# Performance work log

Measured on AMD Instinct MI355X. Metric: run time of the kernel, lower is better.

The kernel has to match this reference:

```python
import jax, jax.numpy as jnp
import numpy as np
import math, functools

QUERY_DIM = 64
HEADS = 4
DIM_HEAD = 16
INNER_DIM = HEADS * DIM_HEAD  # 64


def setup_inputs() -> dict:
    key = jax.random.key(0)
    k0, k1, k2, k3, k4, k5 = jax.random.split(key, 6)
    B, N, H = 4, 4096, 8
    s = 1.0 / math.sqrt(QUERY_DIM)
    return {
        "x": jax.random.normal(k0, (B, N, H, QUERY_DIM), dtype=jnp.float32),
        "Wq": jax.random.normal(k1, (QUERY_DIM, INNER_DIM), dtype=jnp.float32) * s,
        "Wk": jax.random.normal(k2, (QUERY_DIM, INNER_DIM), dtype=jnp.float32) * s,
        "Wv": jax.random.normal(k3, (QUERY_DIM, INNER_DIM), dtype=jnp.float32) * s,
        "Wo": jax.random.normal(k4, (INNER_DIM, QUERY_DIM), dtype=jnp.float32) * s,
        "bo": jnp.zeros((QUERY_DIM,), dtype=jnp.float32),
    }


def _query_chunk_size(n: int) -> int:
    # mirrors the module's chunk-size selection on flatten_latent_dim = shape[-3]
    if n % 64 == 0:
        return n // 64
    if n % 16 == 0:
        return n // 16
    if n % 4 == 0:
        return n // 4
    return n


def _chunked_attention(q, k, v, q_chunk):
    # q,k,v: (..., seq, h, d). Online-softmax chunking over queries; key_chunk_size
    # (16384) exceeds num_kv so a single key chunk is used -> per-q-chunk softmax
    # over the full key axis, which is exactly the same math as the original
    # max-rescaled accumulation.
    prec = jax.lax.Precision.HIGHEST
    scale = 1.0 / math.sqrt(k.shape[-1])
    q = q * scale
    nq = q.shape[-3]

    @functools.partial(jax.checkpoint, prevent_cse=False)
    def one_chunk(i):
        qc = jax.lax.dynamic_slice_in_dim(q, i, q_chunk, axis=-3)  # (..., qc, h, d)
        s = jnp.einsum('...qhd,...khd->...qhk', qc, k, precision=prec)
        a = jax.nn.softmax(s, axis=-1)  # stable: single max-subtract
        return jnp.einsum('...khf,...qhk->...qhf', v, a, precision=prec)

    res = jax.lax.map(one_chunk, jnp.arange(0, nq, q_chunk))  # (nchunks, ..., qc, h, f)
    return jnp.concatenate(res, axis=-3)  # (..., nq, h, f)


def reference(x, Wq, Wk, Wv, Wo, bo):
    # context = x (self-attention path)
    q = jnp.einsum('...d,df->...f', x, Wq)
    k = jnp.einsum('...d,df->...f', x, Wk)
    v = jnp.einsum('...d,df->...f', x, Wv)
    qcs = _query_chunk_size(q.shape[-3])
    hidden = _chunked_attention(q, k, v, qcs)
    return jnp.einsum('...f,fd->...d', hidden, Wo) + bo
```

## Files before the change

### kernel.cpp

```cpp
#include <hip/hip_runtime.h>
#include <hip/hip_bf16.h>

typedef __attribute__((ext_vector_type(8))) short short8;
typedef __attribute__((ext_vector_type(4))) float f32x4;
typedef __attribute__((ext_vector_type(8))) unsigned short ushort8;
typedef __attribute__((ext_vector_type(2))) unsigned uint2v;

#define LOG2E 1.44269504088896340736f

__device__ __forceinline__ float fexp2(float x) {
#if __has_builtin(__builtin_amdgcn_exp2f)
  return __builtin_amdgcn_exp2f(x);
#else
  return exp2f(x);
#endif
}
__device__ __forceinline__ unsigned cvtpk(float lo, float hi) {
  unsigned r;
  asm("v_cvt_pk_bf16_f32 %0, %1, %2" : "=v"(r) : "v"(lo), "v"(hi));
  return r;
}
__device__ __forceinline__ void pswap32(unsigned &a, unsigned &b) {
#if __has_builtin(__builtin_amdgcn_permlane32_swap)
  uint2v r = __builtin_amdgcn_permlane32_swap(a, b, false, false);
  a = r[0]; b = r[1];
#else
  asm("v_permlane32_swap_b32 %0, %1" : "+v"(a), "+v"(b));
#endif
}
__device__ __forceinline__ void gload_lds16(const unsigned short* g, unsigned short* l) {
  __builtin_amdgcn_global_load_lds(
      (const __attribute__((address_space(1))) unsigned int*)g,
      (__attribute__((address_space(3))) unsigned int*)l, 16, 0, 0);
}
__device__ __forceinline__ int swzK(int r) {
  return ((r & 3) | (((r >> 3) & 1) << 2)) << 3;
}

__global__ __launch_bounds__(256) void proj_kernel(
    const float* __restrict__ x,
    const float* __restrict__ Wq, const float* __restrict__ Wk,
    const float* __restrict__ Wv,
    unsigned short* __restrict__ Qo, unsigned short* __restrict__ Ko,
    unsigned short* __restrict__ Vto)
{
  const int tid = threadIdx.x, lane = tid & 63, w = tid >> 6;
  const int r15 = lane & 15, G = lane >> 4;
  const int bh = blockIdx.x >> 4, nt = blockIdx.x & 15;
  const int b = bh >> 3, h = bh & 7;
  const int n0 = nt * 256 + w * 64;

  short8 xf[4][2];
  #pragma unroll
  for (int ct = 0; ct < 4; ++ct) {
    const int n = n0 + ct * 16 + r15;
    const float* xr = x + ((size_t)((b * 4096 + n) * 8 + h)) * 64;
    #pragma unroll
    for (int s = 0; s < 2; ++s) {
      const f32x4 f0 = *(const f32x4*)&xr[s * 32 + G * 8];
      const f32x4 f1 = *(const f32x4*)&xr[s * 32 + G * 8 + 4];
      union { unsigned u[4]; short8 s8; } uu;
      uu.u[0] = cvtpk(f0[0], f0[1]); uu.u[1] = cvtpk(f0[2], f0[3]);
      uu.u[2] = cvtpk(f1[0], f1[1]); uu.u[3] = cvtpk(f1[2], f1[3]);
      xf[ct][s] = uu.s8;
    }
  }

  const size_t obase = (size_t)bh * (4096 * 64);

  #pragma unroll
  for (int wi = 0; wi < 2; ++wi) {
    const float* W = wi ? Wk : Wq;
    unsigned short* O = wi ? Ko : Qo;
    const float sc = wi ? 1.0f : 0.125f * LOG2E;
    short8 wf[4][2];
    #pragma unroll
    for (int ft = 0; ft < 4; ++ft)
      #pragma unroll
      for (int s = 0; s < 2; ++s) {
        union { unsigned u[4]; short8 s8; } uu;
        #pragma unroll
        for (int jj = 0; jj < 4; ++jj) {
          const int k0 = s * 32 + G * 8 + jj * 2;
          uu.u[jj] = cvtpk(W[k0 * 64 + ft * 16 + r15] * sc,
                           W[(k0 + 1) * 64 + ft * 16 + r15] * sc);
        }
        wf[ft][s] = uu.s8;
      }
    f32x4 acc[4][4];
    #pragma unroll
    for (int ft = 0; ft < 4; ++ft)
      #pragma unroll
      for (int ct = 0; ct < 4; ++ct) acc[ft][ct] = (f32x4){0.f, 0.f, 0.f, 0.f};
    #pragma unroll
    for (int s = 0; s < 2; ++s)
      #pragma unroll
      for (int ft = 0; ft < 4; ++ft)
        #pragma unroll
        for (int ct = 0; ct < 4; ++ct)
          acc[ft][ct] = __builtin_amdgcn_mfma_f32_16x16x32_bf16(
              wf[ft][s], xf[ct][s], acc[ft][ct], 0, 0, 0);
    #pragma unroll
    for (int ft = 0; ft < 4; ++ft)
      #pragma unroll
      for (int ct = 0; ct < 4; ++ct) {
        uint2v pk;
        pk[0] = cvtpk(acc[ft][ct][0], acc[ft][ct][1]);
        pk[1] = cvtpk(acc[ft][ct][2], acc[ft][ct][3]);
        *(uint2v*)&O[obase + (size_t)(n0 + ct * 16 + r15) * 64 + ft * 16 + G * 4] = pk;
      }
  }

  {
    short8 wf[4][2];
    #pragma unroll
    for (int ft = 0; ft < 4; ++ft)
      #pragma unroll
      for (int s = 0; s < 2; ++s) {
        union { unsigned u[4]; short8 s8; } uu;
        #pragma unroll
        for (int jj = 0; jj < 4; ++jj) {
          const int k0 = s * 32 + G * 8 + jj * 2;
          uu.u[jj] = cvtpk(Wv[k0 * 64 + ft * 16 + r15], Wv[(k0 + 1) * 64 + ft * 16 + r15]);
        }
        wf[ft][s] = uu.s8;
      }
    f32x4 acc[4][4];
    #pragma unroll
    for (int ct = 0; ct < 4; ++ct)
      #pragma unroll
      for (int ft = 0; ft < 4; ++ft) acc[ct][ft] = (f32x4){0.f, 0.f, 0.f, 0.f};
    #pragma unroll
    for (int s = 0; s < 2; ++s)
      #pragma unroll
      for (int ct = 0; ct < 4; ++ct)
        #pragma unroll
        for (int ft = 0; ft < 4; ++ft)
          acc[ct][ft] = __builtin_amdgcn_mfma_f32_16x16x32_bf16(
              xf[ct][s], wf[ft][s], acc[ct][ft], 0, 0, 0);
    #pragma unroll
    for (int ct = 0; ct < 4; ++ct)
      #pragma unroll
      for (int ft = 0; ft < 4; ++ft) {
        uint2v pk;
        pk[0] = cvtpk(acc[ct][ft][0], acc[ct][ft][1]);
        pk[1] = cvtpk(acc[ct][ft][2], acc[ct][ft][3]);
        *(uint2v*)&Vto[obase + (size_t)(ft * 16 + r15) * 4096 + n0 + ct * 16 + G * 4] = pk;
      }
  }
}

__global__ __launch_bounds__(256, 4) void attn_kernel(
    const unsigned short* __restrict__ Q, const unsigned short* __restrict__ K,
    const unsigned short* __restrict__ Vt, const float* __restrict__ Wo,
    const float* __restrict__ bo, float* __restrict__ out)
{
  __shared__ __align__(16) unsigned short SM[16384];

  const int tid = threadIdx.x;
  const int lane = tid & 63, w = tid >> 6;
  const int r15 = lane & 15, G = lane >> 4;

  int bid = blockIdx.x;
  bid = (bid & 7) * 128 + (bid >> 3);
  const int bh = bid >> 5, qt128 = bid & 31;

  const unsigned short* Qb = Q + (size_t)bh * (4096 * 64);
  const unsigned short* Kb = K + (size_t)bh * (4096 * 64);
  const unsigned short* Vb = Vt + (size_t)bh * (64 * 4096);
  const int q0w = qt128 * 128 + w * 32;

  short8 qf[2][2];
  #pragma unroll
  for (int qt = 0; qt < 2; ++qt) {
    const unsigned short* qr = Qb + (size_t)(q0w + qt * 16 + r15) * 64;
    qf[qt][0] = *(const short8*)&qr[G * 8];
    qf[qt][1] = *(const short8*)&qr[32 + G * 8];
  }

  short8 ones8;
  {
    union { unsigned short us[8]; short8 s8; } o;
    #pragma unroll
    for (int i = 0; i < 8; ++i) o.us[i] = 0x3F80;
    ones8 = o.s8;
  }

  f32x4 oacc[2][4];
  #pragma unroll
  for (int qt = 0; qt < 2; ++qt)
    #pragma unroll
    for (int t = 0; t < 4; ++t) oacc[qt][t] = (f32x4){0.f, 0.f, 0.f, 0.f};
  f32x4 lacc[2];
  lacc[0] = (f32x4){0.f, 0.f, 0.f, 0.f};
  lacc[1] = (f32x4){0.f, 0.f, 0.f, 0.f};

  int kro[4][2], vro[4][2];
  {
    const int Rr = r15 >> 2, gg = r15 & 3;
    #pragma unroll
    for (int t = 0; t < 4; ++t) {
      const int row = gg + ((t & 1) << 2) + ((Rr & 1) << 3) + ((t >> 1) << 4) + ((Rr >> 1) << 5);
      const int sw = swzK(row);
      kro[t][0] = row * 64 + ((G * 8) ^ sw);
      kro[t][1] = row * 64 + ((32 + G * 8) ^ sw);
      const int vrow = t * 16 + r15;
      const int vs = (vrow & 7) << 3;
      vro[t][0] = vrow * 64 + ((G * 8) ^ vs);
      vro[t][1] = vrow * 64 + ((32 + G * 8) ^ vs);
    }
  }

  const int seg = w * 2;
  const int kr0 = seg * 8 + (lane >> 3), kr1 = kr0 + 8;
  const int c8 = (lane & 7) * 8;
  const int koff0 = kr0 * 64 + (c8 ^ swzK(kr0));
  const int koff1 = kr1 * 64 + (c8 ^ swzK(kr1));
  const int voff0 = kr0 * 4096 + (c8 ^ ((kr0 & 7) << 3));
  const int voff1 = kr1 * 4096 + (c8 ^ ((kr1 & 7) << 3));

  gload_lds16(Kb + koff0, &SM[seg * 512]);
  gload_lds16(Kb + koff1, &SM[(seg + 1) * 512]);
  gload_lds16(Vb + voff0, &SM[8192 + seg * 512]);
  gload_lds16(Vb + voff1, &SM[8192 + (seg + 1) * 512]);
  __syncthreads();

  auto TILE = [&](int bufc, int ktc) {
    if (ktc < 63) {
      const int ko = (ktc + 1) * 4096;
      const int vo = (ktc + 1) * 64;
      unsigned short* kd = &SM[(bufc ^ 1) * 4096];
      unsigned short* vd = &SM[8192 + (bufc ^ 1) * 4096];
      gload_lds16(Kb + ko + koff0, kd + seg * 512);
      gload_lds16(Kb + ko + koff1, kd + (seg + 1) * 512);
      gload_lds16(Vb + vo + voff0, vd + seg * 512);
      gload_lds16(Vb + vo + voff1, vd + (seg + 1) * 512);
    }

    const unsigned short* Kc = &SM[bufc * 4096];
    const unsigned short* Vc = &SM[8192 + bufc * 4096];

    f32x4 s[2][4];
    #pragma unroll
    for (int t = 0; t < 4; ++t) {
      const short8 kf0 = *(const short8*)&Kc[kro[t][0]];
      const short8 kf1 = *(const short8*)&Kc[kro[t][1]];
      f32x4 z0 = (f32x4){0.f, 0.f, 0.f, 0.f};
      f32x4 z1 = (f32x4){0.f, 0.f, 0.f, 0.f};
      z0 = __builtin_amdgcn_mfma_f32_16x16x32_bf16(kf0, qf[0][0], z0, 0, 0, 0);
      s[0][t] = __builtin_amdgcn_mfma_f32_16x16x32_bf16(kf1, qf[0][1], z0, 0, 0, 0);
      z1 = __builtin_amdgcn_mfma_f32_16x16x32_bf16(kf0, qf[1][0], z1, 0, 0, 0);
      s[1][t] = __builtin_amdgcn_mfma_f32_16x16x32_bf16(kf1, qf[1][1], z1, 0, 0, 0);
    }

    short8 pa[2][2];
    #pragma unroll
    for (int qt = 0; qt < 2; ++qt) {
      float p[4][4];
      #pragma unroll
      for (int t = 0; t < 4; ++t)
        #pragma unroll
        for (int g = 0; g < 4; ++g) p[t][g] = fexp2(s[qt][t][g]);

      unsigned wA[4], wB[4];
      wA[0] = cvtpk(p[0][0], p[0][1]); wA[1] = cvtpk(p[0][2], p[0][3]);
      wA[2] = cvtpk(p[1][0], p[1][1]); wA[3] = cvtpk(p[1][2], p[1][3]);
      wB[0] = cvtpk(p[2][0], p[2][1]); wB[1] = cvtpk(p[2][2], p[2][3]);
      wB[2] = cvtpk(p[3][0], p[3][1]); wB[3] = cvtpk(p[3][2], p[3][3]);
      union { unsigned u[4]; short8 s8; } fa, fb;
      #pragma unroll
      for (int i = 0; i < 4; ++i) {
        pswap32(wA[i], wB[i]);
        fa.u[i] = wA[i];
        fb.u[i] = wB[i];
      }
      pa[qt][0] = fa.s8;
      pa[qt][1] = fb.s8;
    }

    lacc[0] = __builtin_amdgcn_mfma_f32_16x16x32_bf16(pa[0][0], ones8, lacc[0], 0, 0, 0);
    lacc[0] = __builtin_amdgcn_mfma_f32_16x16x32_bf16(pa[0][1], ones8, lacc[0], 0, 0, 0);
    lacc[1] = __builtin_amdgcn_mfma_f32_16x16x32_bf16(pa[1][0], ones8, lacc[1], 0, 0, 0);
    lacc[1] = __builtin_amdgcn_mfma_f32_16x16x32_bf16(pa[1][1], ones8, lacc[1], 0, 0, 0);

    #pragma unroll
    for (int t = 0; t < 4; ++t) {
      const short8 vb0 = *(const short8*)&Vc[vro[t][0]];
      const short8 vb1 = *(const short8*)&Vc[vro[t][1]];
      oacc[0][t] = __builtin_amdgcn_mfma_f32_16x16x32_bf16(pa[0][0], vb0, oacc[0][t], 0, 0, 0);
      oacc[0][t] = __builtin_amdgcn_mfma_f32_16x16x32_bf16(pa[0][1], vb1, oacc[0][t], 0, 0, 0);
      oacc[1][t] = __builtin_amdgcn_mfma_f32_16x16x32_bf16(pa[1][0], vb0, oacc[1][t], 0, 0, 0);
      oacc[1][t] = __builtin_amdgcn_mfma_f32_16x16x32_bf16(pa[1][1], vb1, oacc[1][t], 0, 0, 0);
    }
    __syncthreads();
  };

  for (int kt = 0; kt < 64; kt += 2) {
    TILE(0, kt);
    TILE(1, kt + 1);
  }

  float* Ol = (float*)&SM[0] + w * 2048;
  #pragma unroll
  for (int qt = 0; qt < 2; ++qt) {
    float li[4];
    #pragma unroll
    for (int g = 0; g < 4; ++g) li[g] = __builtin_amdgcn_rcpf(lacc[qt][g]);
    #pragma unroll
    for (int t = 0; t < 4; ++t)
      #pragma unroll
      for (int g = 0; g < 4; ++g) {
        const int q = qt * 16 + G * 4 + g;
        const int d = t * 16 + r15;
        Ol[q * 64 + (d ^ ((q & 7) << 3))] = oacc[qt][t][g] * li[g];
      }
  }

  short8 wof[4][2];
  #pragma unroll
  for (int nt = 0; nt < 4; ++nt)
    #pragma unroll
    for (int st = 0; st < 2; ++st) {
      union { unsigned u[4]; short8 s8; } uu;
      #pragma unroll
      for (int jj = 0; jj < 4; ++jj) {
        const int k0 = st * 32 + G * 8 + jj * 2;
        uu.u[jj] = cvtpk(Wo[k0 * 64 + nt * 16 + r15], Wo[(k0 + 1) * 64 + nt * 16 + r15]);
      }
      wof[nt][st] = uu.s8;
    }
  float bov[4];
  #pragma unroll
  for (int nt = 0; nt < 4; ++nt) bov[nt] = bo[nt * 16 + r15];

  const int b = bh >> 3, hh = bh & 7;
  #pragma unroll
  for (int qt2 = 0; qt2 < 2; ++qt2) {
    short8 af[2];
    #pragma unroll
    for (int st = 0; st < 2; ++st) {
      const int row = qt2 * 16 + r15;
      const int c = (st * 32 + G * 8) ^ ((row & 7) << 3);
      const f32x4 f0 = *(const f32x4*)&Ol[row * 64 + c];
      const f32x4 f1 = *(const f32x4*)&Ol[row * 64 + c + 4];
      union { unsigned u[4]; short8 s8; } uu;
      uu.u[0] = cvtpk(f0[0], f0[1]); uu.u[1] = cvtpk(f0[2], f0[3]);
      uu.u[2] = cvtpk(f1[0], f1[1]); uu.u[3] = cvtpk(f1[2], f1[3]);
      af[st] = uu.s8;
    }
    #pragma unroll
    for (int nt = 0; nt < 4; ++nt) {
      f32x4 dacc = (f32x4){bov[nt], bov[nt], bov[nt], bov[nt]};
      dacc = __builtin_amdgcn_mfma_f32_16x16x32_bf16(af[0], wof[nt][0], dacc, 0, 0, 0);
      dacc = __builtin_amdgcn_mfma_f32_16x16x32_bf16(af[1], wof[nt][1], dacc, 0, 0, 0);
      #pragma unroll
      for (int g = 0; g < 4; ++g) {
        const int nq = q0w + qt2 * 16 + G * 4 + g;
        out[((size_t)(b * 4096 + nq) * 8 + hh) * 64 + nt * 16 + r15] = dacc[g];
      }
    }
  }
}

extern "C" void kernel_launch(void* const* d_in, const int* in_sizes, int n_in,
                              void* d_out, int out_size, void* d_ws, size_t ws_size,
                              hipStream_t stream) {
  const float* x  = (const float*)d_in[0];
  const float* Wq = (const float*)d_in[1];
  const float* Wk = (const float*)d_in[2];
  const float* Wv = (const float*)d_in[3];
  const float* Wo = (const float*)d_in[4];
  const float* bo = (const float*)d_in[5];

  const size_t NE = 8388608;
  unsigned short* Qw  = (unsigned short*)d_ws;
  unsigned short* Kw  = Qw + NE;
  unsigned short* Vtw = Kw + NE;

  proj_kernel<<<512, 256, 0, stream>>>(x, Wq, Wk, Wv, Qw, Kw, Vtw);
  attn_kernel<<<1024, 256, 0, stream>>>(Qw, Kw, Vtw, Wo, bo, (float*)d_out);
}
```

Measured before the change: 173.3 us.

## Switch attention inner loop to 32x32x16 MFMA tiles with new LDS swizzle

Rewrites the attention kernel's QK^T, row-sum and PV matmuls to use 32x32x16 bf16 MFMA instructions instead of 16x16x32, with each wave handling a full 32-query tile. The K layout swizzle and fragment offsets are redone to match the new operand layout, and launch bounds drop from 4 to 3 waves per SIMD to allow the larger 16-float accumulators. The aim is fewer MFMA issues and LDS reads per tile, traded against higher register pressure and lower occupancy.

```diff
diff --git a/kernel.cpp b/kernel.cpp
--- a/kernel.cpp
+++ b/kernel.cpp
@@ -3,6 +3,7 @@
 
 typedef __attribute__((ext_vector_type(8))) short short8;
 typedef __attribute__((ext_vector_type(4))) float f32x4;
+typedef __attribute__((ext_vector_type(16))) float f32x16;
 typedef __attribute__((ext_vector_type(8))) unsigned short ushort8;
 typedef __attribute__((ext_vector_type(2))) unsigned uint2v;
 
@@ -32,9 +33,6 @@
   __builtin_amdgcn_global_load_lds(
       (const __attribute__((address_space(1))) unsigned int*)g,
       (__attribute__((address_space(3))) unsigned int*)l, 16, 0, 0);
-}
-__device__ __forceinline__ int swzK(int r) {
-  return ((r & 3) | (((r >> 3) & 1) << 2)) << 3;
 }
 
 __global__ __launch_bounds__(256) void proj_kernel(
@@ -150,7 +148,7 @@
   }
 }
 
-__global__ __launch_bounds__(256, 4) void attn_kernel(
+__global__ __launch_bounds__(256, 3) void attn_kernel(
     const unsigned short* __restrict__ Q, const unsigned short* __restrict__ K,
     const unsigned short* __restrict__ Vt, const float* __restrict__ Wo,
     const float* __restrict__ bo, float* __restrict__ out)
@@ -159,6 +157,7 @@
 
   const int tid = threadIdx.x;
   const int lane = tid & 63, w = tid >> 6;
+  const int l31 = lane & 31, hi = lane >> 5;
   const int r15 = lane & 15, G = lane >> 4;
 
   int bid = blockIdx.x;
@@ -170,12 +169,11 @@
   const unsigned short* Vb = Vt + (size_t)bh * (64 * 4096);
   const int q0w = qt128 * 128 + w * 32;
 
-  short8 qf[2][2];
-  #pragma unroll
-  for (int qt = 0; qt < 2; ++qt) {
-    const unsigned short* qr = Qb + (size_t)(q0w + qt * 16 + r15) * 64;
-    qf[qt][0] = *(const short8*)&qr[G * 8];
-    qf[qt][1] = *(const short8*)&qr[32 + G * 8];
+  short8 qf[4];
+  {
+    const unsigned short* qr = Qb + (size_t)(q0w + l31) * 64;
+    #pragma unroll
+    for (int s = 0; s < 4; ++s) qf[s] = *(const short8*)&qr[s * 16 + hi * 8];
   }
 
   short8 ones8;
@@ -186,36 +184,23 @@
     ones8 = o.s8;
   }
 
-  f32x4 oacc[2][4];
-  #pragma unroll
-  for (int qt = 0; qt < 2; ++qt)
-    #pragma unroll
-    for (int t = 0; t < 4; ++t) oacc[qt][t] = (f32x4){0.f, 0.f, 0.f, 0.f};
-  f32x4 lacc[2];
-  lacc[0] = (f32x4){0.f, 0.f, 0.f, 0.f};
-  lacc[1] = (f32x4){0.f, 0.f, 0.f, 0.f};
-
-  int kro[4][2], vro[4][2];
+  f32x16 oacc[2];
+  f32x16 lacc;
+  #pragma unroll
+  for (int r = 0; r < 16; ++r) { oacc[0][r] = 0.f; oacc[1][r] = 0.f; lacc[r] = 0.f; }
+
+  int roffE[4];
   {
-    const int Rr = r15 >> 2, gg = r15 & 3;
-    #pragma unroll
-    for (int t = 0; t < 4; ++t) {
-      const int row = gg + ((t & 1) << 2) + ((Rr & 1) << 3) + ((t >> 1) << 4) + ((Rr >> 1) << 5);
-      const int sw = swzK(row);
-      kro[t][0] = row * 64 + ((G * 8) ^ sw);
-      kro[t][1] = row * 64 + ((32 + G * 8) ^ sw);
-      const int vrow = t * 16 + r15;
-      const int vs = (vrow & 7) << 3;
-      vro[t][0] = vrow * 64 + ((G * 8) ^ vs);
-      vro[t][1] = vrow * 64 + ((32 + G * 8) ^ vs);
-    }
+    const int m = hi ^ (l31 & 7);
+    #pragma unroll
+    for (int s = 0; s < 4; ++s) roffE[s] = l31 * 64 + ((s * 2) ^ m) * 8;
   }
 
   const int seg = w * 2;
   const int kr0 = seg * 8 + (lane >> 3), kr1 = kr0 + 8;
   const int c8 = (lane & 7) * 8;
-  const int koff0 = kr0 * 64 + (c8 ^ swzK(kr0));
-  const int koff1 = kr1 * 64 + (c8 ^ swzK(kr1));
+  const int koff0 = kr0 * 64 + (c8 ^ ((kr0 & 7) << 3));
+  const int koff1 = kr1 * 64 + (c8 ^ ((kr1 & 7) << 3));
   const int voff0 = kr0 * 4096 + (c8 ^ ((kr0 & 7) << 3));
   const int voff1 = kr1 * 4096 + (c8 ^ ((kr1 & 7) << 3));
 
@@ -240,58 +225,43 @@
     const unsigned short* Kc = &SM[bufc * 4096];
     const unsigned short* Vc = &SM[8192 + bufc * 4096];
 
-    f32x4 s[2][4];
-    #pragma unroll
-    for (int t = 0; t < 4; ++t) {
-      const short8 kf0 = *(const short8*)&Kc[kro[t][0]];
-      const short8 kf1 = *(const short8*)&Kc[kro[t][1]];
-      f32x4 z0 = (f32x4){0.f, 0.f, 0.f, 0.f};
-      f32x4 z1 = (f32x4){0.f, 0.f, 0.f, 0.f};
-      z0 = __builtin_amdgcn_mfma_f32_16x16x32_bf16(kf0, qf[0][0], z0, 0, 0, 0);
-      s[0][t] = __builtin_amdgcn_mfma_f32_16x16x32_bf16(kf1, qf[0][1], z0, 0, 0, 0);
-      z1 = __builtin_amdgcn_mfma_f32_16x16x32_bf16(kf0, qf[1][0], z1, 0, 0, 0);
-      s[1][t] = __builtin_amdgcn_mfma_f32_16x16x32_bf16(kf1, qf[1][1], z1, 0, 0, 0);
-    }
-
-    short8 pa[2][2];
-    #pragma unroll
-    for (int qt = 0; qt < 2; ++qt) {
-      float p[4][4];
-      #pragma unroll
-      for (int t = 0; t < 4; ++t)
-        #pragma unroll
-        for (int g = 0; g < 4; ++g) p[t][g] = fexp2(s[qt][t][g]);
-
-      unsigned wA[4], wB[4];
-      wA[0] = cvtpk(p[0][0], p[0][1]); wA[1] = cvtpk(p[0][2], p[0][3]);
-      wA[2] = cvtpk(p[1][0], p[1][1]); wA[3] = cvtpk(p[1][2], p[1][3]);
-      wB[0] = cvtpk(p[2][0], p[2][1]); wB[1] = cvtpk(p[2][2], p[2][3]);
-      wB[2] = cvtpk(p[3][0], p[3][1]); wB[3] = cvtpk(p[3][2], p[3][3]);
-      union { unsigned u[4]; short8 s8; } fa, fb;
-      #pragma unroll
-      for (int i = 0; i < 4; ++i) {
-        pswap32(wA[i], wB[i]);
-        fa.u[i] = wA[i];
-        fb.u[i] = wB[i];
-      }
-      pa[qt][0] = fa.s8;
-      pa[qt][1] = fb.s8;
-    }
-
-    lacc[0] = __builtin_amdgcn_mfma_f32_16x16x32_bf16(pa[0][0], ones8, lacc[0], 0, 0, 0);
-    lacc[0] = __builtin_amdgcn_mfma_f32_16x16x32_bf16(pa[0][1], ones8, lacc[0], 0, 0, 0);
-    lacc[1] = __builtin_amdgcn_mfma_f32_16x16x32_bf16(pa[1][0], ones8, lacc[1], 0, 0, 0);
-    lacc[1] = __builtin_amdgcn_mfma_f32_16x16x32_bf16(pa[1][1], ones8, lacc[1], 0, 0, 0);
-
-    #pragma unroll
-    for (int t = 0; t < 4; ++t) {
-      const short8 vb0 = *(const short8*)&Vc[vro[t][0]];
-      const short8 vb1 = *(const short8*)&Vc[vro[t][1]];
-      oacc[0][t] = __builtin_amdgcn_mfma_f32_16x16x32_bf16(pa[0][0], vb0, oacc[0][t], 0, 0, 0);
-      oacc[0][t] = __builtin_amdgcn_mfma_f32_16x16x32_bf16(pa[0][1], vb1, oacc[0][t], 0, 0, 0);
-      oacc[1][t] = __builtin_amdgcn_mfma_f32_16x16x32_bf16(pa[1][0], vb0, oacc[1][t], 0, 0, 0);
-      oacc[1][t] = __builtin_amdgcn_mfma_f32_16x16x32_bf16(pa[1][1], vb1, oacc[1][t], 0, 0, 0);
-    }
+    short8 pa[4];
+    #pragma unroll
+    for (int kt32 = 0; kt32 < 2; ++kt32) {
+      f32x16 sk;
+      #pragma unroll
+      for (int r = 0; r < 16; ++r) sk[r] = 0.f;
+      #pragma unroll
+      for (int s = 0; s < 4; ++s) {
+        const short8 kf = *(const short8*)&Kc[kt32 * 2048 + roffE[s]];
+        sk = __builtin_amdgcn_mfma_f32_32x32x16_bf16(kf, qf[s], sk, 0, 0, 0);
+      }
+      float p[16];
+      #pragma unroll
+      for (int r = 0; r < 16; ++r) p[r] = fexp2(sk[r]);
+      unsigned wv[8];
+      #pragma unroll
+      for (int i = 0; i < 8; ++i) wv[i] = cvtpk(p[2 * i], p[2 * i + 1]);
+      pswap32(wv[0], wv[2]); pswap32(wv[1], wv[3]);
+      pswap32(wv[4], wv[6]); pswap32(wv[5], wv[7]);
+      union { unsigned u[4]; short8 s8; } f0, f1;
+      f0.u[0] = wv[0]; f0.u[1] = wv[1]; f0.u[2] = wv[2]; f0.u[3] = wv[3];
+      f1.u[0] = wv[4]; f1.u[1] = wv[5]; f1.u[2] = wv[6]; f1.u[3] = wv[7];
+      pa[2 * kt32 + 0] = f0.s8;
+      pa[2 * kt32 + 1] = f1.s8;
+    }
+
+    #pragma unroll
+    for (int s = 0; s < 4; ++s)
+      lacc = __builtin_amdgcn_mfma_f32_32x32x16_bf16(pa[s], ones8, lacc, 0, 0, 0);
+
+    #pragma unroll
+    for (int dt = 0; dt < 2; ++dt)
+      #pragma unroll
+      for (int s = 0; s < 4; ++s) {
+        const short8 vb = *(const short8*)&Vc[dt * 2048 + roffE[s]];
+        oacc[dt] = __builtin_amdgcn_mfma_f32_32x32x16_bf16(pa[s], vb, oacc[dt], 0, 0, 0);
+      }
     __syncthreads();
   };
 
@@ -302,19 +272,13 @@
 
   float* Ol = (float*)&SM[0] + w * 2048;
   #pragma unroll
-  for (int qt = 0; qt < 2; ++qt) {
-    float li[4];
-    #pragma unroll
-    for (int g = 0; g < 4; ++g) li[g] = __builtin_amdgcn_rcpf(lacc[qt][g]);
-    #pragma unroll
-    for (int t = 0; t < 4; ++t)
-      #pragma unroll
-      for (int g = 0; g < 4; ++g) {
-        const int q = qt * 16 + G * 4 + g;
-        const int d = t * 16 + r15;
-        Ol[q * 64 + (d ^ ((q & 7) << 3))] = oacc[qt][t][g] * li[g];
-      }
-  }
+  for (int dt = 0; dt < 2; ++dt)
+    #pragma unroll
+    for (int r = 0; r < 16; ++r) {
+      const int q = (r & 3) + 8 * (r >> 2) + 4 * hi;
+      const int d = dt * 32 + l31;
+      Ol[q * 64 + (d ^ ((q & 7) << 3))] = oacc[dt][r] * __builtin_amdgcn_rcpf(lacc[r]);
+    }
 
   short8 wof[4][2];
   #pragma unroll
```

Result: slower. 194.6 us (+12.3%).
